# Kernel optimization log

Measured on AMD Instinct MI355X. Metric: run time of the kernel, lower is better.

The kernel has to match this reference:

```python
import jax, jax.numpy as jnp
import numpy as np

KS = 3      # kernel size
PAD = 1     # zero padding
STRIDE = 1
N = KS * KS # 9 sampling points per pixel


def _deform_conv(feature, offset, weight):
    """DeformConv2d: bilinear sample at learned offsets then 3x3 conv (no bias)."""
    b, c, h, w = feature.shape
    x = jnp.pad(feature, ((0, 0), (0, 0), (PAD, PAD), (PAD, PAD)))
    hp, wp = h + 2 * PAD, w + 2 * PAD
    dt = feature.dtype
    # p_n: kernel grid offsets, x(rows) first then y(cols) -> (2N,)
    rng = jnp.arange(-(KS - 1) // 2, (KS - 1) // 2 + 1, dtype=dt)
    pn_x, pn_y = jnp.meshgrid(rng, rng, indexing='ij')
    # p_0: base sampling grid starting at 1 (accounts for zero padding)
    p0_x, p0_y = jnp.meshgrid(jnp.arange(1, h + 1, dtype=dt),
                              jnp.arange(1, w + 1, dtype=dt), indexing='ij')
    # sampling locations p = p_0 + p_n + offset, split into x/y -> (b,h,w,N)
    off = jnp.transpose(offset, (0, 2, 3, 1))  # (b,h,w,2N)
    px = p0_x[None, :, :, None] + pn_x.reshape(-1)[None, None, None, :] + off[..., :N]
    py = p0_y[None, :, :, None] + pn_y.reshape(-1)[None, None, None, :] + off[..., N:]
    q_lt_x = jnp.clip(jnp.floor(px), 0, hp - 1)
    q_lt_y = jnp.clip(jnp.floor(py), 0, wp - 1)
    q_rb_x = jnp.clip(jnp.floor(px) + 1, 0, hp - 1)
    q_rb_y = jnp.clip(jnp.floor(py) + 1, 0, wp - 1)
    px = jnp.clip(px, 0, hp - 1)
    py = jnp.clip(py, 0, wp - 1)
    # bilinear weights for the 4 corners
    g_lt = (1 + (q_lt_x - px)) * (1 + (q_lt_y - py))
    g_rb = (1 - (q_rb_x - px)) * (1 - (q_rb_y - py))
    g_lb = (1 + (q_lt_x - px)) * (1 - (q_rb_y - py))
    g_rt = (1 - (q_rb_x - px)) * (1 + (q_lt_y - py))
    x_flat = x.reshape(b, c, hp * wp)

    def gather(qx, qy):
        idx = (qx * wp + qy).astype(jnp.int32).reshape(b, 1, -1)
        v = jnp.take_along_axis(x_flat, jnp.broadcast_to(idx, (b, c, h * w * N)), axis=2)
        return v.reshape(b, c, h, w, N)

    x_off = (g_lt[:, None] * gather(q_lt_x, q_lt_y)
             + g_rb[:, None] * gather(q_rb_x, q_rb_y)
             + g_lb[:, None] * gather(q_lt_x, q_rb_y)
             + g_rt[:, None] * gather(q_rb_x, q_lt_y))  # (b,c,h,w,N)
    # equivalent of _reshape_x_offset + conv(ks, stride=ks)
    x_off = x_off.reshape(b, c, h, w, KS, KS)
    return jnp.einsum('bchwij,ocij->bohw', x_off, weight)


def setup_inputs() -> dict:
    key = jax.random.key(0)
    k1, k2, k3 = jax.random.split(key, 3)
    B, C, H, W = 4, 256, 64, 64
    feature = jax.random.normal(k1, (B, C, H, W), dtype=jnp.float32)
    offset = jax.random.normal(k2, (B, 2 * N, H, W), dtype=jnp.float32)
    weight = jax.random.normal(k3, (C, C, KS, KS), dtype=jnp.float32) / np.sqrt(C * N)
    return {"feature": feature, "offset": offset, "weight": weight}


def reference(feature, offset, weight):
    f1 = jax.nn.relu(_deform_conv(feature, offset, weight))
    return jax.nn.relu(f1 + feature)
```

## Files before the change

kernel.cpp:

```cpp
#include <hip/hip_runtime.h>

#define HW    4096
#define J_TOT 16384
#define K_TOT 2304
#define C_CH  256

typedef unsigned short u16;
typedef unsigned int   u32;
typedef __attribute__((ext_vector_type(8))) short short8;
typedef __attribute__((ext_vector_type(4))) float f32x4;
typedef __attribute__((ext_vector_type(4))) unsigned short us4;

__device__ __forceinline__ float b2f(u16 u) { return __uint_as_float(((u32)u) << 16); }
__device__ __forceinline__ u16 f2b(float x) {
  u32 u = __float_as_uint(x);
  u += 0x7FFFu + ((u >> 16) & 1u);
  return (u16)(u >> 16);
}

__device__ __forceinline__ void gload_lds16(const u16* g, u16* l) {
  __builtin_amdgcn_global_load_lds(
      (__attribute__((address_space(1))) void*)(void*)g,
      (__attribute__((address_space(3))) void*)(void*)l, 16, 0, 0);
}

__global__ void k_detect(const u16* __restrict__ f, int* __restrict__ flag) {
  __shared__ int sh[256];
  int t = threadIdx.x;
  int hits = 0;
  for (int i = t; i < 2048; i += 256) {
    u16 u = f[2 * i];
    int e = (u >> 7) & 0xFF;
    hits += (e >= 100 && e <= 141) ? 1 : 0;
  }
  sh[t] = hits;
  __syncthreads();
  if (t == 0) {
    int s = 0;
    for (int i = 0; i < 256; i++) s += sh[i];
    flag[0] = (s > 1024) ? 1 : 0;
  }
}

__global__ void k_prep(const void* __restrict__ featv, u16* __restrict__ ftr,
                       const void* __restrict__ wv, u16* __restrict__ Wr,
                       const int* __restrict__ flag, int isbf_h) {
  int isbf = (isbf_h >= 0) ? isbf_h : *flag;
  int tx = threadIdx.x;
  int ty = threadIdx.y;
  int z = blockIdx.z;
  if (z < 4) {
    __shared__ u16 tile[32][33];
    int b = z;
    int hw0 = blockIdx.x << 5;
    int c0 = blockIdx.y << 5;
    if (isbf) {
      const u16* f = (const u16*)featv;
#pragma unroll
      for (int i = 0; i < 4; i++) {
        int c = c0 + ty + i * 8;
        tile[ty + i * 8][tx] = f[(((size_t)(b * C_CH + c)) << 12) + hw0 + tx];
      }
    } else {
      const float* f = (const float*)featv;
#pragma unroll
      for (int i = 0; i < 4; i++) {
        int c = c0 + ty + i * 8;
        tile[ty + i * 8][tx] = f2b(f[(((size_t)(b * C_CH + c)) << 12) + hw0 + tx]);
      }
    }
    __syncthreads();
#pragma unroll
    for (int i = 0; i < 4; i++) {
      int hw = hw0 + ty + i * 8;
      ftr[(((size_t)(b * HW + hw)) << 8) + c0 + tx] = tile[tx][ty + i * 8];
    }
  } else {
    __shared__ u16 wtile[2304];
    int bid = blockIdx.x + (blockIdx.y << 7);
    if (bid >= C_CH) return;
    int flat = ty * 32 + tx;
    if (isbf) {
      const u16* wsrc = (const u16*)wv + (size_t)bid * K_TOT;
      for (int i = flat; i < K_TOT; i += 256) wtile[i] = wsrc[i];
    } else {
      const float* wsrc = (const float*)wv + (size_t)bid * K_TOT;
      for (int i = flat; i < K_TOT; i += 256) wtile[i] = f2b(wsrc[i]);
    }
    __syncthreads();
    u16* wdst = Wr + (size_t)bid * K_TOT;
#pragma unroll
    for (int n = 0; n < 9; n++) wdst[n * 256 + flat] = wtile[flat * 9 + n];
  }
}

#define NT 36

#define A_DMA(Ab)                                                            \
  do {                                                                       \
    gload_lds16(asrc0, (Ab) + wave * 1024);                                  \
    gload_lds16(asrc1, (Ab) + wave * 1024 + 512);                            \
    asrc0 += 64; asrc1 += 64;                                                \
  } while (0)

#define PLOAD_S(tile, P)                                                     \
  do {                                                                       \
    if (((tile) & 3) == 0) {                                                 \
      int np_ = (tile) >> 2;                                                 \
      tw0 = gs[np_][0][pp]; tw1 = gs[np_][1][pp];                            \
      tw2 = gs[np_][2][pp]; tw3 = gs[np_][3][pp];                            \
      ti0 = isx[np_][0][pp]; ti1 = isx[np_][1][pp];                          \
      ti2 = isx[np_][2][pp]; ti3 = isx[np_][3][pp];                          \
    }                                                                        \
    int c0_ = (((tile) & 3) << 6) + cb4;                                     \
    P##w0 = tw0; P##w1 = tw1; P##w2 = tw2; P##w3 = tw3;                      \
    P##q0 = *(const us4*)(ftr + ti0 + c0_);                                  \
    P##q1 = *(const us4*)(ftr + ti1 + c0_);                                  \
    P##q2 = *(const us4*)(ftr + ti2 + c0_);                                  \
    P##q3 = *(const us4*)(ftr + ti3 + c0_);                                  \
  } while (0)

#define PFIN_S(P, Bb)                                                        \
  do {                                                                       \
    us4 ov;                                                                  \
    _Pragma("unroll")                                                        \
    for (int i = 0; i < 4; i++) {                                            \
      float v = P##w0 * b2f(P##q0[i]) + P##w1 * b2f(P##q1[i]) +              \
                P##w2 * b2f(P##q2[i]) + P##w3 * b2f(P##q3[i]);               \
      ov[i] = f2b(v);                                                        \
    }                                                                        \
    *(us4*)((Bb) + bofs) = ov;                                               \
  } while (0)

#define GEMM_COMPUTE(Ab, Bb)                                                 \
  do {                                                                       \
    short8 af[2][2], bf[2][2];                                               \
    _Pragma("unroll")                                                        \
    for (int kk = 0; kk < 2; kk++) {                                         \
      int go = (((kk << 2) + lk) ^ swz) << 3;                                \
      _Pragma("unroll")                                                      \
      for (int oi = 0; oi < 2; oi++)                                         \
        af[oi][kk] = *(const short8*)((Ab) + (wo * 32 + oi * 16 + lr) * 64 + go); \
      _Pragma("unroll")                                                      \
      for (int ji = 0; ji < 2; ji++)                                         \
        bf[ji][kk] = *(const short8*)((Bb) + (wj * 32 + ji * 16 + lr) * 64 + go); \
    }                                                                        \
    __builtin_amdgcn_s_setprio(1);                                           \
    _Pragma("unroll")                                                        \
    for (int kk = 0; kk < 2; kk++)                                           \
      _Pragma("unroll")                                                      \
      for (int oi = 0; oi < 2; oi++)                                         \
        _Pragma("unroll")                                                    \
        for (int ji = 0; ji < 2; ji++)                                       \
          acc[oi][ji] = __builtin_amdgcn_mfma_f32_16x16x32_bf16(             \
              af[oi][kk], bf[ji][kk], acc[oi][ji], 0, 0, 0);                 \
    __builtin_amdgcn_s_setprio(0);                                           \
  } while (0)

#define CBAR()                                                               \
  do {                                                                       \
    asm volatile("s_waitcnt vmcnt(6) lgkmcnt(0)" ::: "memory");              \
    __builtin_amdgcn_s_barrier();                                            \
  } while (0)

#define ROTATE()                                                             \
  do {                                                                       \
    u16* tp_ = Ac; Ac = An; An = Af; Af = tp_;                               \
    tp_ = Bc; Bc = Bn; Bn = Bf; Bf = tp_;                                    \
  } while (0)

__device__ __forceinline__ void gemm_body(const u16* __restrict__ Wr,
                                          const u16* __restrict__ ftr,
                                          const void* __restrict__ offv,
                                          const void* __restrict__ featv,
                                          void* __restrict__ outv,
                                          const int isbf) {
  __shared__ u16 As[3][256 * 64];
  __shared__ u16 Bs[3][64 * 64];
  __shared__ float gs[9][4][64];
  __shared__ int   isx[9][4][64];
  int bid = blockIdx.x;
  int xb = (bid & 7) * 32 + (bid >> 3);
  int j0 = xb << 6;
  int b = j0 >> 12;
  int hw0 = j0 & (HW - 1);
  int t = threadIdx.x;
  int wave = t >> 6, lane = t & 63;
  int wj = wave >> 3, wo = wave & 7;
  int lr = lane & 15, lk = lane >> 4;
  int swz = lr & 7;

  if (t < 576) {
    int n = t >> 6, p = t & 63;
    int hw = hw0 + p;
    int h = hw >> 6, w = hw & 63;
    size_t obi = (((size_t)(b * 18 + n)) << 12) + hw;
    float ox, oy;
    if (isbf) {
      const u16* po = (const u16*)offv;
      ox = b2f(po[obi]);
      oy = b2f(po[obi + (9u << 12)]);
    } else {
      const float* po = (const float*)offv;
      ox = po[obi];
      oy = po[obi + (9u << 12)];
    }
    int ki = n / 3, kj = n % 3;
    float px = (float)(h + ki) + ox;
    float py = (float)(w + kj) + oy;
    float fx = floorf(px), fy = floorf(py);
    float qltx = fminf(fmaxf(fx, 0.f), 65.f);
    float qlty = fminf(fmaxf(fy, 0.f), 65.f);
    float qrbx = fminf(fmaxf(fx + 1.f, 0.f), 65.f);
    float qrby = fminf(fmaxf(fy + 1.f, 0.f), 65.f);
    float pcx = fminf(fmaxf(px, 0.f), 65.f);
    float pcy = fminf(fmaxf(py, 0.f), 65.f);
    float dltx = 1.f + (qltx - pcx);
    float drbx = 1.f - (qrbx - pcx);
    float dlty = 1.f + (qlty - pcy);
    float drby = 1.f - (qrby - pcy);
    float g0 = dltx * dlty;
    float g1 = drbx * drby;
    float g2 = dltx * drby;
    float g3 = drbx * dlty;
    int x0 = (int)qltx, y0 = (int)qlty, x1 = (int)qrbx, y1 = (int)qrby;
    int v0 = (x0 >= 1 && x0 <= 64 && y0 >= 1 && y0 <= 64);
    int v1 = (x1 >= 1 && x1 <= 64 && y1 >= 1 && y1 <= 64);
    int v2 = (x0 >= 1 && x0 <= 64 && y1 >= 1 && y1 <= 64);
    int v3 = (x1 >= 1 && x1 <= 64 && y0 >= 1 && y0 <= 64);
    int base = b << 12;
    isx[n][0][p] = v0 ? ((base + ((x0 - 1) << 6) + (y0 - 1)) << 8) : 0;
    isx[n][1][p] = v1 ? ((base + ((x1 - 1) << 6) + (y1 - 1)) << 8) : 0;
    isx[n][2][p] = v2 ? ((base + ((x0 - 1) << 6) + (y1 - 1)) << 8) : 0;
    isx[n][3][p] = v3 ? ((base + ((x1 - 1) << 6) + (y0 - 1)) << 8) : 0;
    gs[n][0][p] = v0 ? g0 : 0.f;
    gs[n][1][p] = v1 ? g1 : 0.f;
    gs[n][2][p] = v2 ? g2 : 0.f;
    gs[n][3][p] = v3 ? g3 : 0.f;
  }

  f32x4 acc[2][2];
  f32x4 zero = {0.f, 0.f, 0.f, 0.f};
#pragma unroll
  for (int i = 0; i < 2; i++)
#pragma unroll
    for (int j = 0; j < 2; j++) acc[i][j] = zero;

  int rb = lane >> 3;
  int cs = ((lane & 7) ^ rb) << 3;
  const u16* asrc0 = Wr + (size_t)(wave * 16 + 0 + rb) * K_TOT + cs;
  const u16* asrc1 = Wr + (size_t)(wave * 16 + 8 + rb) * K_TOT + cs;

  int pp = t >> 4, qq = t & 15;
  int cgp = qq >> 1, half = qq & 1;
  int bofs = pp * 64 + ((cgp ^ (pp & 7)) << 3) + (half << 2);
  int cb4 = (cgp << 3) + (half << 2);

  u16 *Ac = &As[0][0], *An = &As[1][0], *Af = &As[2][0];
  u16 *Bc = &Bs[0][0], *Bn = &Bs[1][0], *Bf = &Bs[2][0];

  __syncthreads();

  us4 aq0, aq1, aq2, aq3, bq0, bq1, bq2, bq3;
  float aw0, aw1, aw2, aw3, bw0, bw1, bw2, bw3;
  float tw0, tw1, tw2, tw3;
  int ti0, ti1, ti2, ti3;

  PLOAD_S(0, a); A_DMA(Ac);
  PFIN_S(a, Bc);
  PLOAD_S(1, b); A_DMA(An);
  CBAR();

#pragma unroll 1
  for (int it = 0; it < 17; ++it) {
    PLOAD_S(2 * it + 2, a);
    A_DMA(Af);
    GEMM_COMPUTE(Ac, Bc);
    PFIN_S(b, Bn);
    CBAR();
    ROTATE();
    PLOAD_S(2 * it + 3, b);
    A_DMA(Af);
    GEMM_COMPUTE(Ac, Bc);
    PFIN_S(a, Bn);
    CBAR();
    ROTATE();
  }
  GEMM_COMPUTE(Ac, Bc);
  PFIN_S(b, Bn);
  asm volatile("s_waitcnt vmcnt(0) lgkmcnt(0)" ::: "memory");
  __builtin_amdgcn_s_barrier();
  GEMM_COMPUTE(An, Bn);

  int lq = lane >> 4;
#pragma unroll
  for (int oi = 0; oi < 2; oi++) {
#pragma unroll
    for (int ji = 0; ji < 2; ji++) {
      int j = j0 + wj * 32 + ji * 16 + lr;
      int bb_ = j >> 12, hw = j & (HW - 1);
      int o0 = wo * 32 + oi * 16 + lq * 4;
#pragma unroll
      for (int r = 0; r < 4; r++) {
        size_t oidx = (((size_t)(bb_ * C_CH + o0 + r)) << 12) + hw;
        float v = acc[oi][ji][r];
        v = fmaxf(v, 0.f);
        float ft = isbf ? b2f(((const u16*)featv)[oidx]) : ((const float*)featv)[oidx];
        v = fmaxf(v + ft, 0.f);
        if (isbf) ((u16*)outv)[oidx] = f2b(v);
        else      ((float*)outv)[oidx] = v;
      }
    }
  }
}

__global__ __launch_bounds__(1024, 4) void k_gemm_f32(const u16* __restrict__ Wr,
                                                      const u16* __restrict__ ftr,
                                                      const void* __restrict__ offv,
                                                      const void* __restrict__ featv,
                                                      void* __restrict__ outv) {
  gemm_body(Wr, ftr, offv, featv, outv, 0);
}

__global__ __launch_bounds__(1024, 4) void k_gemm_bf16(const u16* __restrict__ Wr,
                                                       const u16* __restrict__ ftr,
                                                       const void* __restrict__ offv,
                                                       const void* __restrict__ featv,
                                                       void* __restrict__ outv) {
  gemm_body(Wr, ftr, offv, featv, outv, 1);
}

__global__ __launch_bounds__(1024, 4) void k_gemm_flag(const u16* __restrict__ Wr,
                                                       const u16* __restrict__ ftr,
                                                       const void* __restrict__ offv,
                                                       const void* __restrict__ featv,
                                                       void* __restrict__ outv,
                                                       const int* __restrict__ flag) {
  int isbf = *flag;
  asm volatile("s_waitcnt vmcnt(0)" ::: "memory");
  gemm_body(Wr, ftr, offv, featv, outv, isbf);
}

extern "C" void kernel_launch(void* const* d_in, const int* in_sizes, int n_in,
                              void* d_out, int out_size, void* d_ws, size_t ws_size,
                              hipStream_t stream) {
  const void* feat = d_in[0];
  const void* offs = d_in[1];
  const void* wght = d_in[2];

  const size_t off_flag = 0;
  const size_t off_wr   = 256;
  const size_t off_ftr  = off_wr + (size_t)1179648;
  const size_t need     = off_ftr + (size_t)8388608;
  if (ws_size < need) return;

  char* ws = (char*)d_ws;
  int* flag = (int*)(ws + off_flag);
  u16* Wr   = (u16*)(ws + off_wr);
  u16* ftr  = (u16*)(ws + off_ftr);

  int isbf_h = -1;
  if (out_size == 16777216) isbf_h = 0;
  else if (out_size == 8388608) isbf_h = 1;
  if (isbf_h < 0 && in_sizes && n_in >= 3) {
    if (in_sizes[0] == 16777216 && in_sizes[2] == 2359296) isbf_h = 0;
    else if (in_sizes[0] == 8388608 && in_sizes[2] == 1179648) isbf_h = 1;
  }
  if (isbf_h < 0)
    k_detect<<<1, 256, 0, stream>>>((const u16*)feat, flag);
  k_prep<<<dim3(128, 8, 5), dim3(32, 8), 0, stream>>>(feat, ftr, wght, Wr, flag, isbf_h);
  if (isbf_h == 0)
    k_gemm_f32<<<J_TOT / 64, 1024, 0, stream>>>(Wr, ftr, offs, feat, d_out);
  else if (isbf_h == 1)
    k_gemm_bf16<<<J_TOT / 64, 1024, 0, stream>>>(Wr, ftr, offs, feat, d_out);
  else
    k_gemm_flag<<<J_TOT / 64, 1024, 0, stream>>>(Wr, ftr, offs, feat, d_out, flag);
}
```

Before: 129.8 us.

## Fuse prep and GEMM into one cooperative kernel with grid sync

Replaces the separate prep (feature transpose and weight reorder) and GEMM launches with a single cooperative kernel of 256 blocks that runs the prep work, does a grid-wide sync, then runs the deformable GEMM body. The aim is to remove a kernel launch and the inter-kernel gap. In exchange it adds a grid barrier and a fixed block-to-job mapping for prep. It also gives up the compile-time dtype specialisation, since isbf is now a runtime value inside the fused kernel. The old multi-kernel path remains as a fallback if the cooperative launch fails.

```diff
diff --git a/kernel.cpp b/kernel.cpp
--- a/kernel.cpp
+++ b/kernel.cpp
@@ -1,4 +1,7 @@
 #include <hip/hip_runtime.h>
+#include <hip/hip_cooperative_groups.h>
+
+namespace cg = cooperative_groups;
 
 #define HW    4096
 #define J_TOT 16384
@@ -22,76 +25,6 @@
   __builtin_amdgcn_global_load_lds(
       (__attribute__((address_space(1))) void*)(void*)g,
       (__attribute__((address_space(3))) void*)(void*)l, 16, 0, 0);
-}
-
-__global__ void k_detect(const u16* __restrict__ f, int* __restrict__ flag) {
-  __shared__ int sh[256];
-  int t = threadIdx.x;
-  int hits = 0;
-  for (int i = t; i < 2048; i += 256) {
-    u16 u = f[2 * i];
-    int e = (u >> 7) & 0xFF;
-    hits += (e >= 100 && e <= 141) ? 1 : 0;
-  }
-  sh[t] = hits;
-  __syncthreads();
-  if (t == 0) {
-    int s = 0;
-    for (int i = 0; i < 256; i++) s += sh[i];
-    flag[0] = (s > 1024) ? 1 : 0;
-  }
-}
-
-__global__ void k_prep(const void* __restrict__ featv, u16* __restrict__ ftr,
-                       const void* __restrict__ wv, u16* __restrict__ Wr,
-                       const int* __restrict__ flag, int isbf_h) {
-  int isbf = (isbf_h >= 0) ? isbf_h : *flag;
-  int tx = threadIdx.x;
-  int ty = threadIdx.y;
-  int z = blockIdx.z;
-  if (z < 4) {
-    __shared__ u16 tile[32][33];
-    int b = z;
-    int hw0 = blockIdx.x << 5;
-    int c0 = blockIdx.y << 5;
-    if (isbf) {
-      const u16* f = (const u16*)featv;
-#pragma unroll
-      for (int i = 0; i < 4; i++) {
-        int c = c0 + ty + i * 8;
-        tile[ty + i * 8][tx] = f[(((size_t)(b * C_CH + c)) << 12) + hw0 + tx];
-      }
-    } else {
-      const float* f = (const float*)featv;
-#pragma unroll
-      for (int i = 0; i < 4; i++) {
-        int c = c0 + ty + i * 8;
-        tile[ty + i * 8][tx] = f2b(f[(((size_t)(b * C_CH + c)) << 12) + hw0 + tx]);
-      }
-    }
-    __syncthreads();
-#pragma unroll
-    for (int i = 0; i < 4; i++) {
-      int hw = hw0 + ty + i * 8;
-      ftr[(((size_t)(b * HW + hw)) << 8) + c0 + tx] = tile[tx][ty + i * 8];
-    }
-  } else {
-    __shared__ u16 wtile[2304];
-    int bid = blockIdx.x + (blockIdx.y << 7);
-    if (bid >= C_CH) return;
-    int flat = ty * 32 + tx;
-    if (isbf) {
-      const u16* wsrc = (const u16*)wv + (size_t)bid * K_TOT;
-      for (int i = flat; i < K_TOT; i += 256) wtile[i] = wsrc[i];
-    } else {
-      const float* wsrc = (const float*)wv + (size_t)bid * K_TOT;
-      for (int i = flat; i < K_TOT; i += 256) wtile[i] = f2b(wsrc[i]);
-    }
-    __syncthreads();
-    u16* wdst = Wr + (size_t)bid * K_TOT;
-#pragma unroll
-    for (int n = 0; n < 9; n++) wdst[n * 256 + flat] = wtile[flat * 9 + n];
-  }
 }
 
 #define NT 36
@@ -314,20 +247,162 @@
   }
 }
 
-__global__ __launch_bounds__(1024, 4) void k_gemm_f32(const u16* __restrict__ Wr,
-                                                      const u16* __restrict__ ftr,
-                                                      const void* __restrict__ offv,
-                                                      const void* __restrict__ featv,
-                                                      void* __restrict__ outv) {
-  gemm_body(Wr, ftr, offv, featv, outv, 0);
-}
-
-__global__ __launch_bounds__(1024, 4) void k_gemm_bf16(const u16* __restrict__ Wr,
-                                                       const u16* __restrict__ ftr,
-                                                       const void* __restrict__ offv,
-                                                       const void* __restrict__ featv,
-                                                       void* __restrict__ outv) {
-  gemm_body(Wr, ftr, offv, featv, outv, 1);
+__device__ __forceinline__ void prep_phase(const void* __restrict__ featv,
+                                           const void* __restrict__ wv,
+                                           u16* __restrict__ ftr,
+                                           u16* __restrict__ Wr,
+                                           const int isbf, const int blk,
+                                           const int t) {
+  __shared__ u16 tile[4][32][33];
+  int sub = t >> 8, tj = t & 255;
+  int tx = tj & 31, ty = tj >> 5;
+#pragma unroll 1
+  for (int it = 0; it < 4; ++it) {
+    int job = blk * 16 + it * 4 + sub;
+    int hw0 = (job & 127) << 5;
+    int c0 = ((job >> 7) & 7) << 5;
+    int b = job >> 10;
+    if (isbf) {
+      const u16* f = (const u16*)featv;
+#pragma unroll
+      for (int i = 0; i < 4; i++) {
+        int c = c0 + ty + i * 8;
+        tile[sub][ty + i * 8][tx] = f[(((size_t)(b * C_CH + c)) << 12) + hw0 + tx];
+      }
+    } else {
+      const float* f = (const float*)featv;
+#pragma unroll
+      for (int i = 0; i < 4; i++) {
+        int c = c0 + ty + i * 8;
+        tile[sub][ty + i * 8][tx] = f2b(f[(((size_t)(b * C_CH + c)) << 12) + hw0 + tx]);
+      }
+    }
+    __syncthreads();
+#pragma unroll
+    for (int i = 0; i < 4; i++) {
+      int hw = hw0 + ty + i * 8;
+      ftr[(((size_t)(b * HW + hw)) << 8) + c0 + tx] = tile[sub][tx][ty + i * 8];
+    }
+    __syncthreads();
+  }
+  __shared__ u16 wtile[2304];
+  if (isbf) {
+    const u16* wsrc = (const u16*)wv + (size_t)blk * K_TOT;
+    for (int i = t; i < K_TOT; i += 1024) wtile[i] = wsrc[i];
+  } else {
+    const float* wsrc = (const float*)wv + (size_t)blk * K_TOT;
+    for (int i = t; i < K_TOT; i += 1024) wtile[i] = f2b(wsrc[i]);
+  }
+  __syncthreads();
+  u16* wdst = Wr + (size_t)blk * K_TOT;
+  for (int k = t; k < K_TOT; k += 1024) wdst[k] = wtile[(k & 255) * 9 + (k >> 8)];
+}
+
+__global__ __launch_bounds__(1024, 4) void k_fused(const void* __restrict__ featv,
+                                                   const void* __restrict__ offv,
+                                                   const void* __restrict__ wv,
+                                                   void* __restrict__ outv,
+                                                   u16* __restrict__ ftr,
+                                                   u16* __restrict__ Wr,
+                                                   int isbf_h) {
+  int t = threadIdx.x;
+  int blk = blockIdx.x;
+  int isbf = isbf_h;
+  if (isbf < 0) {
+    __shared__ int dsum;
+    if (t == 0) dsum = 0;
+    __syncthreads();
+    if (t < 256) {
+      const u16* f = (const u16*)featv;
+      int hits = 0;
+      for (int i = t; i < 2048; i += 256) {
+        u16 u = f[2 * i];
+        int e = (u >> 7) & 0xFF;
+        hits += (e >= 100 && e <= 141) ? 1 : 0;
+      }
+      atomicAdd(&dsum, hits);
+    }
+    __syncthreads();
+    isbf = (dsum > 1024) ? 1 : 0;
+  }
+
+  prep_phase(featv, wv, ftr, Wr, isbf, blk, t);
+
+  __threadfence();
+  cg::this_grid().sync();
+  asm volatile("s_waitcnt vmcnt(0) lgkmcnt(0)" ::: "memory");
+
+  gemm_body(Wr, ftr, offv, featv, outv, isbf);
+}
+
+__global__ void k_detect(const u16* __restrict__ f, int* __restrict__ flag) {
+  __shared__ int sh[256];
+  int t = threadIdx.x;
+  int hits = 0;
+  for (int i = t; i < 2048; i += 256) {
+    u16 u = f[2 * i];
+    int e = (u >> 7) & 0xFF;
+    hits += (e >= 100 && e <= 141) ? 1 : 0;
+  }
+  sh[t] = hits;
+  __syncthreads();
+  if (t == 0) {
+    int s = 0;
+    for (int i = 0; i < 256; i++) s += sh[i];
+    flag[0] = (s > 1024) ? 1 : 0;
+  }
+}
+
+__global__ void k_prep(const void* __restrict__ featv, u16* __restrict__ ftr,
+                       const void* __restrict__ wv, u16* __restrict__ Wr,
+                       const int* __restrict__ flag) {
+  int isbf = *flag;
+  int tx = threadIdx.x;
+  int ty = threadIdx.y;
+  int z = blockIdx.z;
+  if (z < 4) {
+    __shared__ u16 tile[32][33];
+    int b = z;
+    int hw0 = blockIdx.x << 5;
+    int c0 = blockIdx.y << 5;
+    if (isbf) {
+      const u16* f = (const u16*)featv;
+#pragma unroll
+      for (int i = 0; i < 4; i++) {
+        int c = c0 + ty + i * 8;
+        tile[ty + i * 8][tx] = f[(((size_t)(b * C_CH + c)) << 12) + hw0 + tx];
+      }
+    } else {
+      const float* f = (const float*)featv;
+#pragma unroll
+      for (int i = 0; i < 4; i++) {
+        int c = c0 + ty + i * 8;
+        tile[ty + i * 8][tx] = f2b(f[(((size_t)(b * C_CH + c)) << 12) + hw0 + tx]);
+      }
+    }
+    __syncthreads();
+#pragma unroll
+    for (int i = 0; i < 4; i++) {
+      int hw = hw0 + ty + i * 8;
+      ftr[(((size_t)(b * HW + hw)) << 8) + c0 + tx] = tile[tx][ty + i * 8];
+    }
+  } else {
+    __shared__ u16 wtile[2304];
+    int bid = blockIdx.x + (blockIdx.y << 7);
+    if (bid >= C_CH) return;
+    int flat = ty * 32 + tx;
+    if (isbf) {
+      const u16* wsrc = (const u16*)wv + (size_t)bid * K_TOT;
+      for (int i = flat; i < K_TOT; i += 256) wtile[i] = wsrc[i];
+    } else {
+      const float* wsrc = (const float*)wv + (size_t)bid * K_TOT;
+      for (int i = flat; i < K_TOT; i += 256) wtile[i] = f2b(wsrc[i]);
+    }
+    __syncthreads();
+    u16* wdst = Wr + (size_t)bid * K_TOT;
+#pragma unroll
+    for (int n = 0; n < 9; n++) wdst[n * 256 + flat] = wtile[flat * 9 + n];
+  }
 }
 
 __global__ __launch_bounds__(1024, 4) void k_gemm_flag(const u16* __restrict__ Wr,
@@ -366,13 +441,18 @@
     if (in_sizes[0] == 16777216 && in_sizes[2] == 2359296) isbf_h = 0;
     else if (in_sizes[0] == 8388608 && in_sizes[2] == 1179648) isbf_h = 1;
   }
-  if (isbf_h < 0)
+
+  void* feat_ = (void*)feat;
+  void* offs_ = (void*)offs;
+  void* wght_ = (void*)wght;
+  void* out_  = d_out;
+  void* args[] = {&feat_, &offs_, &wght_, &out_, &ftr, &Wr, &isbf_h};
+  hipError_t err = hipLaunchCooperativeKernel(
+      reinterpret_cast<void*>(k_fused), dim3(256), dim3(1024), args, 0, stream);
+
+  if (err != hipSuccess) {
     k_detect<<<1, 256, 0, stream>>>((const u16*)feat, flag);
-  k_prep<<<dim3(128, 8, 5), dim3(32, 8), 0, stream>>>(feat, ftr, wght, Wr, flag, isbf_h);
-  if (isbf_h == 0)
-    k_gemm_f32<<<J_TOT / 64, 1024, 0, stream>>>(Wr, ftr, offs, feat, d_out);
-  else if (isbf_h == 1)
-    k_gemm_bf16<<<J_TOT / 64, 1024, 0, stream>>>(Wr, ftr, offs, feat, d_out);
-  else
+    k_prep<<<dim3(128, 8, 5), dim3(32, 8), 0, stream>>>(feat, ftr, wght, Wr, flag);
     k_gemm_flag<<<J_TOT / 64, 1024, 0, stream>>>(Wr, ftr, offs, feat, d_out, flag);
-}
+  }
+}
```

After: 228.3 us. 1.76x slower.
